# Kernel tuning notes

Measured on AMD Instinct MI355X. Metric: run time of the kernel, lower is better.

## Reference

```python
import jax, jax.numpy as jnp
import numpy as np
import math

D = 1024      # d_model
K = 64        # k_eigenstates
H = 4         # n_heads
KH = K // H   # eigenstates per head
MLP = 4 * D
B, T = 4, 4096


def setup_inputs() -> dict:
    key = jax.random.key(0)
    ks = jax.random.split(key, 16)
    rn = lambda k, shape, s: (jax.random.normal(k, shape, jnp.float32) * s)
    inp = {
        "x": rn(ks[0], (B, T, D), 1.0),
        "W_in": rn(ks[1], (2 * K, D), 1.0 / math.sqrt(D)),
        "log_decay": jax.random.uniform(ks[2], (K,), jnp.float32, -3.0, -0.1),
        "frequency": jnp.linspace(0.0, 2 * math.pi * (1 - 1.0 / K), K, dtype=jnp.float32),
        "W_sel": rn(ks[3], (2 * K, D), 0.01 / math.sqrt(D)),
        "b_sel": jnp.zeros((2 * K,), jnp.float32),
        "R": jnp.eye(KH, dtype=jnp.float32)[None] + 0.01 * rn(ks[4], (H, KH, KH), 1.0 / math.sqrt(KH)),
        "W_out": rn(ks[5], (D, 2 * K), 1.0 / math.sqrt(2 * K)),
        "W_g": rn(ks[6], (D, D), 1.0 / math.sqrt(D)),
        "b_g": jnp.full((D,), -2.0, jnp.float32),
        "g1": jnp.ones((D,), jnp.float32),
        "be1": jnp.zeros((D,), jnp.float32),
        "g2": jnp.ones((D,), jnp.float32),
        "be2": jnp.zeros((D,), jnp.float32),
        "W1": rn(ks[7], (MLP, D), 1.0 / math.sqrt(D)),
        "b1": jnp.zeros((MLP,), jnp.float32),
        "W2": rn(ks[8], (D, MLP), 1.0 / math.sqrt(MLP)),
        "b2": jnp.zeros((D,), jnp.float32),
    }
    return inp


def _ln(x, g, b):
    m = jnp.mean(x, axis=-1, keepdims=True)
    v = jnp.mean(jnp.square(x - m), axis=-1, keepdims=True)
    return (x - m) * jax.lax.rsqrt(v + 1e-5) * g + b


def _scan_combine(e1, e2):
    a1, b1 = e1
    a2, b2 = e2
    return a1 * a2, a2 * b1 + b2


def reference(x, W_in, log_decay, frequency, W_sel, b_sel, R, W_out, W_g, b_g,
              g1, be1, g2, be2, W1, b1, W2, b2):
    Bsz, Ts, Dm = x.shape
    residual = x
    x_norm = _ln(x, g1, be1)

    beta = x_norm @ W_in.T                      # [B,T,2K]
    beta_r, beta_i = jnp.split(beta, 2, axis=-1)

    delta = x_norm @ W_sel.T + b_sel            # selective modulation
    d_dec, d_fr = jnp.split(delta, 2, axis=-1)
    mag = jax.nn.sigmoid(log_decay + 0.1 * jnp.tanh(d_dec))   # [B,T,K]
    freq = frequency + 0.05 * jnp.tanh(d_fr)

    a = jax.lax.complex(mag * jnp.cos(freq), mag * jnp.sin(freq))  # lambda_t
    bc = jax.lax.complex(beta_r, beta_i)
    # inclusive prefix scan of c_t = a_t * c_{t-1} + b_t
    _, c = jax.lax.associative_scan(_scan_combine, (a, bc), axis=1)
    c_r, c_i = c.real, c.imag                   # [B,T,K]

    nH, Kh = R.shape[0], R.shape[1]
    c_r = jnp.einsum('hjk,bthk->bthj', R, c_r.reshape(Bsz, Ts, nH, Kh)).reshape(Bsz, Ts, -1)
    c_i = jnp.einsum('hjk,bthk->bthj', R, c_i.reshape(Bsz, Ts, nH, Kh)).reshape(Bsz, Ts, -1)

    h = jnp.concatenate([c_r, c_i], axis=-1) @ W_out.T
    gate = jax.nn.sigmoid(x_norm @ W_g.T + b_g)
    x = residual + gate * h

    x2 = _ln(x, g2, be2)
    x = x + (jax.nn.silu(x2 @ W1.T + b1) @ W2.T + b2)
    return x
```

## Files before the change

### kernel.cpp

```cpp
#include <hip/hip_runtime.h>
#include <math.h>

typedef __bf16 bf16_t;
typedef __attribute__((ext_vector_type(8))) __bf16 bf16x8;
typedef __attribute__((ext_vector_type(4))) float f32x4;

#define DMODEL 1024
#define NROWS  16384
#define SEQLEN 4096

static __device__ __forceinline__ float sigmoidf_(float v) { return 1.f / (1.f + __expf(-v)); }

#define GLOAD16(gsrc, ldst) __builtin_amdgcn_global_load_lds(                     \
    (const __attribute__((address_space(1))) void*)(gsrc),                        \
    (__attribute__((address_space(3))) void*)(ldst), 16, 0, 0)

__global__ __launch_bounds__(256) void ln_fused_kernel(const float* __restrict__ x,
                                                       const float* __restrict__ g,
                                                       const float* __restrict__ b,
                                                       bf16_t* __restrict__ out) {
  int row = blockIdx.x;
  int tid = threadIdx.x;
  const float4* xr = (const float4*)(x + (size_t)row * DMODEL);
  float4 v = xr[tid];
  float s  = v.x + v.y + v.z + v.w;
  float s2 = v.x*v.x + v.y*v.y + v.z*v.z + v.w*v.w;
  #pragma unroll
  for (int off = 32; off > 0; off >>= 1) {
    s  += __shfl_down(s, off);
    s2 += __shfl_down(s2, off);
  }
  __shared__ float sh[4], sh2[4];
  int lane = tid & 63, wid = tid >> 6;
  if (lane == 0) { sh[wid] = s; sh2[wid] = s2; }
  __syncthreads();
  s  = sh[0] + sh[1] + sh[2] + sh[3];
  s2 = sh2[0] + sh2[1] + sh2[2] + sh2[3];
  float m = s * (1.f / DMODEL);
  float var = fmaxf(s2 * (1.f / DMODEL) - m * m, 0.f);
  float rs = rsqrtf(var + 1e-5f);
  float4 gv = *(const float4*)&g[tid * 4];
  float4 bv = *(const float4*)&b[tid * 4];
  union { bf16_t h[4]; float2 f2; } u;
  u.h[0] = (bf16_t)((v.x - m) * rs * gv.x + bv.x);
  u.h[1] = (bf16_t)((v.y - m) * rs * gv.y + bv.y);
  u.h[2] = (bf16_t)((v.z - m) * rs * gv.z + bv.z);
  u.h[3] = (bf16_t)((v.w - m) * rs * gv.w + bv.w);
  *(float2*)&out[(size_t)row * DMODEL + tid * 4] = u.f2;
}

__global__ __launch_bounds__(256) void f32_to_bf16_kernel(const float* __restrict__ in,
                                                          bf16_t* __restrict__ out, int n) {
  int idx = (blockIdx.x * 256 + threadIdx.x) * 4;
  if (idx >= n) return;
  float4 v = *(const float4*)&in[idx];
  union { bf16_t h[4]; float2 f2; } u;
  u.h[0] = (bf16_t)v.x; u.h[1] = (bf16_t)v.y; u.h[2] = (bf16_t)v.z; u.h[3] = (bf16_t)v.w;
  *(float2*)&out[idx] = u.f2;
}

template<int EPI>
__global__ __launch_bounds__(512, 2) void gemm256_kernel(
    const bf16_t* __restrict__ A, int lda,
    const bf16_t* __restrict__ B, int ldb, int K, int nx,
    const float* __restrict__ bias,
    const float* __restrict__ res,
    const float* __restrict__ aux,
    float* __restrict__ outf, bf16_t* __restrict__ outb, int ldout) {
  __shared__ __align__(1024) char lds[2][2][32768];
  const int nwg = gridDim.x;
  const int bid = blockIdx.x;
  const int lid = (bid & 7) * (nwg >> 3) + (bid >> 3);
  const int n0 = (lid % nx) * 256;
  const int r0 = (lid / nx) * 256;

  const int tid = threadIdx.x;
  const int lane = tid & 63;
  const int w = tid >> 6;
  const int wr = w >> 2, wc = w & 3;
  const int fr = lane & 15;
  const int q16m = ((lane >> 4) * 16) ^ (((lane >> 2) & 1) << 5);
  const int srow = w * 8 + (lane >> 3);
  const int scolb = ((lane & 7) * 16) ^ (lane & 32);

  f32x4 acc[8][4];
  #pragma unroll
  for (int m = 0; m < 8; ++m)
    #pragma unroll
    for (int n = 0; n < 4; ++n) acc[m][n] = (f32x4){0.f, 0.f, 0.f, 0.f};

  const int nt = K >> 6;

  auto stage = [&](int d, int k0) {
    #pragma unroll
    for (int i = 0; i < 4; ++i) {
      GLOAD16((const char*)(A + (size_t)(r0 + i * 64 + srow) * lda + k0) + scolb,
              lds[d][0] + i * 8192 + w * 1024);
      GLOAD16((const char*)(B + (size_t)(n0 + i * 64 + srow) * ldb + k0) + scolb,
              lds[d][1] + i * 8192 + w * 1024);
    }
  };

  auto compute = [&](int d) {
    bf16x8 bfrag[4][2];
    #pragma unroll
    for (int n = 0; n < 4; ++n) {
      const char* bp = lds[d][1] + (wc * 64 + n * 16 + fr) * 128 + q16m;
      bfrag[n][0] = *(const bf16x8*)bp;
      bfrag[n][1] = *(const bf16x8*)(bp + 64);
    }
    #pragma unroll
    for (int mh = 0; mh < 2; ++mh) {
      bf16x8 afrag[4][2];
      #pragma unroll
      for (int m = 0; m < 4; ++m) {
        const char* ap = lds[d][0] + (wr * 128 + mh * 64 + m * 16 + fr) * 128 + q16m;
        afrag[m][0] = *(const bf16x8*)ap;
        afrag[m][1] = *(const bf16x8*)(ap + 64);
      }
      #pragma unroll
      for (int m = 0; m < 4; ++m)
        #pragma unroll
        for (int n = 0; n < 4; ++n) {
          acc[mh * 4 + m][n] = __builtin_amdgcn_mfma_f32_16x16x32_bf16(afrag[m][0], bfrag[n][0], acc[mh * 4 + m][n], 0, 0, 0);
          acc[mh * 4 + m][n] = __builtin_amdgcn_mfma_f32_16x16x32_bf16(afrag[m][1], bfrag[n][1], acc[mh * 4 + m][n], 0, 0, 0);
        }
    }
  };

  stage(0, 0);
  __syncthreads();
  for (int t = 0; t < nt; ++t) {
    if (t + 1 < nt) stage((t + 1) & 1, (t + 1) << 6);
    compute(t & 1);
    __syncthreads();
  }

  const int rbase = (lane >> 4) * 4;
  #pragma unroll
  for (int mf = 0; mf < 8; ++mf) {
    #pragma unroll
    for (int n = 0; n < 4; ++n) {
      int row = r0 + wr * 128 + mf * 16 + rbase;
      int col = n0 + wc * 64 + n * 16 + fr;
      f32x4 v = acc[mf][n];
      #pragma unroll
      for (int j = 0; j < 4; ++j) {
        int r = row + j;
        float val = v[j];
        if (EPI == 0) {
          outf[(size_t)r * ldout + col] = val;
        } else if (EPI == 1) {
          float t2 = val + bias[col];
          t2 = t2 * sigmoidf_(t2);
          outb[(size_t)r * ldout + col] = (bf16_t)t2;
        } else if (EPI == 2) {
          outf[(size_t)r * ldout + col] = res[(size_t)r * 1024 + col] + bias[col] + val;
        } else if (EPI == 3) {
          outf[(size_t)r * ldout + col] += val;
        } else {
          size_t idx = (size_t)r * 1024 + col;
          outf[idx] = res[idx] + sigmoidf_(val + bias[col]) * aux[idx];
        }
      }
    }
  }
}

template<int EPI>
__global__ __launch_bounds__(256) void gemm_bf16_kernel(
    const bf16_t* __restrict__ A, int lda,
    const bf16_t* __restrict__ B, int ldb, int K, int nx,
    float* __restrict__ outf, int ldout) {
  __shared__ __align__(16) bf16_t As[128 * 32];
  __shared__ __align__(16) bf16_t Bs[128 * 32];
  const int nwg = gridDim.x;
  const int bid = blockIdx.x;
  const int lid = (bid & 7) * (nwg >> 3) + (bid >> 3);
  const int n0 = (lid % nx) * 128;
  const int r0 = (lid / nx) * 128;

  const int tid = threadIdx.x;
  const int lane = tid & 63;
  const int w = tid >> 6;
  const int wr = w >> 1, wc = w & 1;
  const int srow0 = tid >> 2;
  const int srow1 = 64 + (tid >> 2);
  const int skk = (tid & 3) * 8;
  const int fr = lane & 15;
  const int ko = (lane >> 4) * 8;

  f32x4 acc[4][4];
  #pragma unroll
  for (int m = 0; m < 4; ++m)
    #pragma unroll
    for (int n = 0; n < 4; ++n) acc[m][n] = (f32x4){0.f, 0.f, 0.f, 0.f};

  for (int k0 = 0; k0 < K; k0 += 32) {
    GLOAD16(A + (size_t)(r0 + srow0) * lda + k0 + skk, (char*)As + w * 1024);
    GLOAD16(A + (size_t)(r0 + srow1) * lda + k0 + skk, (char*)As + 4096 + w * 1024);
    GLOAD16(B + (size_t)(n0 + srow0) * ldb + k0 + skk, (char*)Bs + w * 1024);
    GLOAD16(B + (size_t)(n0 + srow1) * ldb + k0 + skk, (char*)Bs + 4096 + w * 1024);
    __syncthreads();
    bf16x8 af[4], bfr[4];
    #pragma unroll
    for (int m = 0; m < 4; ++m)
      af[m] = *(const bf16x8*)&As[(wr * 64 + m * 16 + fr) * 32 + ko];
    #pragma unroll
    for (int n = 0; n < 4; ++n)
      bfr[n] = *(const bf16x8*)&Bs[(wc * 64 + n * 16 + fr) * 32 + ko];
    #pragma unroll
    for (int m = 0; m < 4; ++m)
      #pragma unroll
      for (int n = 0; n < 4; ++n)
        acc[m][n] = __builtin_amdgcn_mfma_f32_16x16x32_bf16(af[m], bfr[n], acc[m][n], 0, 0, 0);
    __syncthreads();
  }

  const int rbase = (lane >> 4) * 4;
  #pragma unroll
  for (int m = 0; m < 4; ++m) {
    #pragma unroll
    for (int n = 0; n < 4; ++n) {
      int row = r0 + wr * 64 + m * 16 + rbase;
      int col = n0 + wc * 64 + n * 16 + fr;
      f32x4 v = acc[m][n];
      #pragma unroll
      for (int j = 0; j < 4; ++j)
        outf[(size_t)(row + j) * ldout + col] = v[j];
    }
  }
}

__global__ __launch_bounds__(256) void ew_ab_kernel(
    const float* __restrict__ bd, const float* __restrict__ b_sel,
    const float* __restrict__ log_decay, const float* __restrict__ frequency,
    float* __restrict__ a_r, float* __restrict__ a_i,
    float* __restrict__ b_r, float* __restrict__ b_i) {
  __shared__ float T[32][257];
  int bb = blockIdx.x >> 7;
  int t0 = (blockIdx.x & 127) << 5;
  int tid = threadIdx.x;
  #pragma unroll
  for (int p = 0; p < 32; ++p) {
    int idx = tid + p * 256;
    int tt = idx >> 8, j = idx & 255;
    T[tt][j] = bd[((size_t)bb * 4096 + t0 + tt) * 256 + j];
  }
  __syncthreads();
  #pragma unroll
  for (int p = 0; p < 8; ++p) {
    int idx = tid + p * 256;
    int tt = idx & 31, k = idx >> 5;
    float br_ = T[tt][k];
    float bi_ = T[tt][64 + k];
    float dd = T[tt][128 + k] + b_sel[k];
    float df = T[tt][192 + k] + b_sel[64 + k];
    float mag = sigmoidf_(log_decay[k] + 0.1f * tanhf(dd));
    float fr = frequency[k] + 0.05f * tanhf(df);
    float ar_ = mag * cosf(fr), ai_ = mag * sinf(fr);
    size_t o = ((size_t)bb * 64 + k) * 4096 + t0 + tt;
    a_r[o] = ar_; a_i[o] = ai_; b_r[o] = br_; b_i[o] = bi_;
  }
}

__global__ __launch_bounds__(256) void scan_kernel(
    const float* __restrict__ a_r, const float* __restrict__ a_i,
    const float* b_r, const float* b_i,
    float* c_r, float* c_i) {
  int seq = blockIdx.x;
  size_t base = (size_t)seq * SEQLEN;
  int tid = threadIdx.x;
  int t0 = tid * 16;
  float Ar = 1.f, Ai = 0.f, Br = 0.f, Bi = 0.f;
  #pragma unroll
  for (int s = 0; s < 16; ++s) {
    size_t t = base + t0 + s;
    float ar = a_r[t], ai = a_i[t], br = b_r[t], bi = b_i[t];
    float nBr = ar * Br - ai * Bi + br;
    float nBi = ar * Bi + ai * Br + bi;
    Br = nBr; Bi = nBi;
    float nAr = ar * Ar - ai * Ai;
    float nAi = ar * Ai + ai * Ar;
    Ar = nAr; Ai = nAi;
  }
  __shared__ float sAr[256], sAi[256], sBr[256], sBi[256];
  sAr[tid] = Ar; sAi[tid] = Ai; sBr[tid] = Br; sBi[tid] = Bi;
  for (int off = 1; off < 256; off <<= 1) {
    __syncthreads();
    float pAr = 0.f, pAi = 0.f, pBr = 0.f, pBi = 0.f;
    if (tid >= off) { pAr = sAr[tid - off]; pAi = sAi[tid - off]; pBr = sBr[tid - off]; pBi = sBi[tid - off]; }
    __syncthreads();
    if (tid >= off) {
      float cAr = sAr[tid], cAi = sAi[tid], cBr = sBr[tid], cBi = sBi[tid];
      float nBr = cAr * pBr - cAi * pBi + cBr;
      float nBi = cAr * pBi + cAi * pBr + cBi;
      float nAr = cAr * pAr - cAi * pAi;
      float nAi = cAr * pAi + cAi * pAr;
      sAr[tid] = nAr; sAi[tid] = nAi; sBr[tid] = nBr; sBi[tid] = nBi;
    }
  }
  __syncthreads();
  float cr = (tid > 0) ? sBr[tid - 1] : 0.f;
  float ci = (tid > 0) ? sBi[tid - 1] : 0.f;
  #pragma unroll
  for (int s = 0; s < 16; ++s) {
    size_t t = base + t0 + s;
    float ar = a_r[t], ai = a_i[t], br = b_r[t], bi = b_i[t];
    float nr = ar * cr - ai * ci + br;
    float ni = ar * ci + ai * cr + bi;
    cr = nr; ci = ni;
    c_r[t] = cr; c_i[t] = ci;
  }
}

__global__ __launch_bounds__(256) void transpose_cc_kernel(
    const float* __restrict__ c_r, const float* __restrict__ c_i,
    bf16_t* __restrict__ cc) {
  __shared__ float Tr[64][65];
  __shared__ float Ti[64][65];
  int t0 = blockIdx.x * 64;
  int bb = blockIdx.y;
  int tid = threadIdx.x;
  int tt = tid & 63;
  int q = tid >> 6;
  #pragma unroll
  for (int p = 0; p < 16; ++p) {
    int k = p * 4 + q;
    size_t src = ((size_t)bb * 64 + k) * 4096 + t0 + tt;
    Tr[tt][k] = c_r[src];
    Ti[tt][k] = c_i[src];
  }
  __syncthreads();
  #pragma unroll
  for (int p = 0; p < 16; ++p) {
    int tt2 = p * 4 + q;
    int k = tid & 63;
    size_t row = (size_t)bb * 4096 + t0 + tt2;
    cc[row * 128 + k] = (bf16_t)Tr[tt2][k];
    cc[row * 128 + 64 + k] = (bf16_t)Ti[tt2][k];
  }
}

__global__ __launch_bounds__(256) void weff_kernel(const float* __restrict__ W_out,
                                                   const float* __restrict__ R,
                                                   bf16_t* __restrict__ Weff) {
  int idx = blockIdx.x * 256 + threadIdx.x;
  int d = idx >> 7, col = idx & 127;
  int k = col & 63, h = k >> 4, kk = k & 15;
  int off = (col < 64) ? 0 : 64;
  float s = 0.f;
  #pragma unroll
  for (int j = 0; j < 16; ++j)
    s += W_out[d * 128 + off + h * 16 + j] * R[h * 256 + j * 16 + kk];
  Weff[idx] = (bf16_t)s;
}

extern "C" void kernel_launch(void* const* d_in, const int* in_sizes, int n_in,
                              void* d_out, int out_size, void* d_ws, size_t ws_size,
                              hipStream_t stream) {
  (void)in_sizes; (void)n_in; (void)out_size; (void)ws_size;
  const float* x         = (const float*)d_in[0];
  const float* W_in      = (const float*)d_in[1];
  const float* log_decay = (const float*)d_in[2];
  const float* frequency = (const float*)d_in[3];
  const float* W_sel     = (const float*)d_in[4];
  const float* b_sel     = (const float*)d_in[5];
  const float* R         = (const float*)d_in[6];
  const float* W_out     = (const float*)d_in[7];
  const float* W_g       = (const float*)d_in[8];
  const float* b_g       = (const float*)d_in[9];
  const float* g1        = (const float*)d_in[10];
  const float* be1       = (const float*)d_in[11];
  const float* g2        = (const float*)d_in[12];
  const float* be2       = (const float*)d_in[13];
  const float* W1        = (const float*)d_in[14];
  const float* b1        = (const float*)d_in[15];
  const float* W2        = (const float*)d_in[16];
  const float* b2        = (const float*)d_in[17];
  float* out = (float*)d_out;
  float* ws  = (float*)d_ws;

  const size_t M1 = (size_t)1 << 20;
  float* bd   = ws;
  float* xmid = ws;
  float* a_r  = ws + 16 * M1;
  float* a_i  = ws + 20 * M1;
  float* b_rr = ws + 24 * M1;
  float* b_ii = ws + 28 * M1;
  float* hbuf = ws + 16 * M1;
  bf16_t* mid = (bf16_t*)(ws + 16 * M1);
  bf16_t* xn  = (bf16_t*)(ws + 32 * M1);
  bf16_t* cc  = (bf16_t*)(ws + 40 * M1);
  bf16_t* Wbd = (bf16_t*)(ws + 41 * M1);
  bf16_t* Wgb = (bf16_t*)(ws + 41 * M1 + (128 << 10));
  bf16_t* W1b = (bf16_t*)(ws + 41 * M1 + (640 << 10));
  bf16_t* W2b = (bf16_t*)(ws + 43 * M1 + (640 << 10));
  bf16_t* Wef = (bf16_t*)(ws + 45 * M1 + (640 << 10));

  dim3 blk(256);
  dim3 blk512(512);

  ln_fused_kernel<<<NROWS, blk, 0, stream>>>(x, g1, be1, xn);

  f32_to_bf16_kernel<<<128, blk, 0, stream>>>(W_in, Wbd, 128 * 1024);
  f32_to_bf16_kernel<<<128, blk, 0, stream>>>(W_sel, Wbd + 128 * 1024, 128 * 1024);
  f32_to_bf16_kernel<<<1024, blk, 0, stream>>>(W_g, Wgb, 1024 * 1024);
  f32_to_bf16_kernel<<<4096, blk, 0, stream>>>(W1, W1b, 4 * 1024 * 1024);
  f32_to_bf16_kernel<<<4096, blk, 0, stream>>>(W2, W2b, 4 * 1024 * 1024);
  weff_kernel<<<512, blk, 0, stream>>>(W_out, R, Wef);

  gemm_bf16_kernel<0><<<256, blk, 0, stream>>>(xn, 1024, Wbd, 1024, 1024, 2, bd, 256);

  ew_ab_kernel<<<512, blk, 0, stream>>>(bd, b_sel, log_decay, frequency, a_r, a_i, b_rr, b_ii);
  scan_kernel<<<256, blk, 0, stream>>>(a_r, a_i, b_rr, b_ii, b_rr, b_ii);
  transpose_cc_kernel<<<dim3(64, 4), blk, 0, stream>>>(b_rr, b_ii, cc);

  gemm256_kernel<0><<<256, blk512, 0, stream>>>(
      cc, 128, Wef, 128, 128, 4, nullptr, nullptr, nullptr, hbuf, nullptr, 1024);

  gemm256_kernel<4><<<256, blk512, 0, stream>>>(
      xn, 1024, Wgb, 1024, 1024, 4, b_g, x, hbuf, xmid, nullptr, 1024);

  ln_fused_kernel<<<NROWS, blk, 0, stream>>>(xmid, g2, be2, xn);

  for (int h = 0; h < 2; ++h) {
    gemm256_kernel<1><<<512, blk512, 0, stream>>>(
        xn, 1024, W1b + (size_t)h * 2048 * 1024, 1024, 1024, 8,
        b1 + h * 2048, nullptr, nullptr, nullptr, mid, 2048);
    if (h == 0) {
      gemm256_kernel<2><<<256, blk512, 0, stream>>>(
          mid, 2048, W2b, 4096, 2048, 4,
          b2, xmid, nullptr, out, nullptr, 1024);
    } else {
      gemm256_kernel<3><<<256, blk512, 0, stream>>>(
          mid, 2048, W2b + 2048, 4096, 2048, 4,
          nullptr, nullptr, nullptr, out, nullptr, 1024);
    }
  }
}
```

Before: 545.0 us.

## Pipeline bf16 GEMM mainloop into four prioritized phases with interleaved LDS staging

Replaces the simple double-buffered stage/compute loop of the 256x256 bf16 GEMM with a four-phase schedule. Each phase loads one A or B quarter-fragment from LDS, issues the next tile's global-to-LDS loads for a freed half, then runs a block of MFMAs at raised wave priority between barriers. Explicit vmcnt/lgkmcnt waits replace the full __syncthreads per tile. The LDS layout and XOR swizzle are also reorganised into per-half buffers. This aims to overlap global loads, LDS reads and MFMA work more finely, at the cost of more barriers and fragile hand-tuned wait counts.

Result: faster. 527.0 us (-3.3%).

```diff
diff --git a/kernel.cpp b/kernel.cpp
--- a/kernel.cpp
+++ b/kernel.cpp
@@ -59,6 +59,43 @@
   *(float2*)&out[idx] = u.f2;
 }
 
+#define LOADA(d, mh)                                                              \
+  { _Pragma("unroll")                                                             \
+    for (int m_ = 0; m_ < 4; ++m_) {                                              \
+      _Pragma("unroll")                                                           \
+      for (int kk_ = 0; kk_ < 2; ++kk_)                                           \
+        afrag[m_][kk_] = *(const bf16x8*)(ldsp + (d) * 32768 + (mh) * 16384 +     \
+            (aRow + m_ * 16) * 128 + ((kk_ * 64 + q16) ^ swz));                   \
+    } }
+
+#define LOADB(d, nn)                                                              \
+  { _Pragma("unroll")                                                             \
+    for (int n2_ = 0; n2_ < 2; ++n2_) {                                           \
+      _Pragma("unroll")                                                           \
+      for (int kk_ = 0; kk_ < 2; ++kk_)                                           \
+        bfrag[nn][n2_][kk_] = *(const bf16x8*)(ldsp + 65536 + (d) * 32768 +       \
+            (nn) * 16384 + (bRow + n2_ * 16) * 128 + ((kk_ * 64 + q16) ^ swz));   \
+    } }
+
+#define MFMAQ(mh, nn)                                                             \
+  { _Pragma("unroll")                                                             \
+    for (int m_ = 0; m_ < 4; ++m_) {                                              \
+      _Pragma("unroll")                                                           \
+      for (int n2_ = 0; n2_ < 2; ++n2_) {                                         \
+        acc[(mh)*4+m_][(nn)*2+n2_] = __builtin_amdgcn_mfma_f32_16x16x32_bf16(     \
+            afrag[m_][0], bfrag[nn][n2_][0], acc[(mh)*4+m_][(nn)*2+n2_], 0,0,0);  \
+        acc[(mh)*4+m_][(nn)*2+n2_] = __builtin_amdgcn_mfma_f32_16x16x32_bf16(     \
+            afrag[m_][1], bfrag[nn][n2_][1], acc[(mh)*4+m_][(nn)*2+n2_], 0,0,0);  \
+      }                                                                           \
+    } }
+
+#define PH_PRE()  __builtin_amdgcn_s_barrier();                                   \
+                  asm volatile("s_waitcnt lgkmcnt(0)");                           \
+                  __builtin_amdgcn_sched_barrier(0);                              \
+                  __builtin_amdgcn_s_setprio(1)
+#define PH_POST() __builtin_amdgcn_s_setprio(0);                                  \
+                  __builtin_amdgcn_s_barrier()
+
 template<int EPI>
 __global__ __launch_bounds__(512, 2) void gemm256_kernel(
     const bf16_t* __restrict__ A, int lda,
@@ -67,7 +104,7 @@
     const float* __restrict__ res,
     const float* __restrict__ aux,
     float* __restrict__ outf, bf16_t* __restrict__ outb, int ldout) {
-  __shared__ __align__(1024) char lds[2][2][32768];
+  __shared__ __align__(128) char ldsp[131072];
   const int nwg = gridDim.x;
   const int bid = blockIdx.x;
   const int lid = (bid & 7) * (nwg >> 3) + (bid >> 3);
@@ -79,61 +116,87 @@
   const int w = tid >> 6;
   const int wr = w >> 2, wc = w & 3;
   const int fr = lane & 15;
-  const int q16m = ((lane >> 4) * 16) ^ (((lane >> 2) & 1) << 5);
-  const int srow = w * 8 + (lane >> 3);
-  const int scolb = ((lane & 7) * 16) ^ (lane & 32);
+  const int q16 = (lane >> 4) * 16;
+  const int swz = (fr & 7) << 4;
+  const int aRow = wr * 64 + fr;
+  const int bRow = wc * 32 + fr;
+
+  const size_t lda_b = (size_t)lda * 2;
+  const size_t ldb_b = (size_t)ldb * 2;
+  const char* Ab = (const char*)A;
+  const char* Bb = (const char*)B;
+  const int trow = tid >> 3;
+  const int scolb = (((tid & 7) ^ (trow & 7)) << 4);
+
+  auto stageA = [&](int d, int h, int kt) {
+    const char* src = Ab + (size_t)(r0 + h * 64 + trow) * lda_b + kt * 128 + scolb;
+    char* dst = ldsp + d * 32768 + h * 16384 + tid * 16;
+    GLOAD16(src, dst);
+    GLOAD16(src + 128 * lda_b, dst + 8192);
+  };
+  auto stageB = [&](int d, int g, int kt) {
+    const int r1 = 64 + trow;
+    const char* s0 = Bb + (size_t)(n0 + (trow >> 5) * 64 + g * 32 + (trow & 31)) * ldb_b + kt * 128 + scolb;
+    const char* s1 = Bb + (size_t)(n0 + (r1 >> 5) * 64 + g * 32 + (r1 & 31)) * ldb_b + kt * 128 + scolb;
+    char* dst = ldsp + 65536 + d * 32768 + g * 16384 + tid * 16;
+    GLOAD16(s0, dst);
+    GLOAD16(s1, dst + 8192);
+  };
 
   f32x4 acc[8][4];
   #pragma unroll
   for (int m = 0; m < 8; ++m)
     #pragma unroll
     for (int n = 0; n < 4; ++n) acc[m][n] = (f32x4){0.f, 0.f, 0.f, 0.f};
+  bf16x8 afrag[4][2];
+  bf16x8 bfrag[2][2][2];
 
   const int nt = K >> 6;
 
-  auto stage = [&](int d, int k0) {
-    #pragma unroll
-    for (int i = 0; i < 4; ++i) {
-      GLOAD16((const char*)(A + (size_t)(r0 + i * 64 + srow) * lda + k0) + scolb,
-              lds[d][0] + i * 8192 + w * 1024);
-      GLOAD16((const char*)(B + (size_t)(n0 + i * 64 + srow) * ldb + k0) + scolb,
-              lds[d][1] + i * 8192 + w * 1024);
-    }
-  };
-
-  auto compute = [&](int d) {
-    bf16x8 bfrag[4][2];
-    #pragma unroll
-    for (int n = 0; n < 4; ++n) {
-      const char* bp = lds[d][1] + (wc * 64 + n * 16 + fr) * 128 + q16m;
-      bfrag[n][0] = *(const bf16x8*)bp;
-      bfrag[n][1] = *(const bf16x8*)(bp + 64);
-    }
-    #pragma unroll
-    for (int mh = 0; mh < 2; ++mh) {
-      bf16x8 afrag[4][2];
-      #pragma unroll
-      for (int m = 0; m < 4; ++m) {
-        const char* ap = lds[d][0] + (wr * 128 + mh * 64 + m * 16 + fr) * 128 + q16m;
-        afrag[m][0] = *(const bf16x8*)ap;
-        afrag[m][1] = *(const bf16x8*)(ap + 64);
-      }
-      #pragma unroll
-      for (int m = 0; m < 4; ++m)
-        #pragma unroll
-        for (int n = 0; n < 4; ++n) {
-          acc[mh * 4 + m][n] = __builtin_amdgcn_mfma_f32_16x16x32_bf16(afrag[m][0], bfrag[n][0], acc[mh * 4 + m][n], 0, 0, 0);
-          acc[mh * 4 + m][n] = __builtin_amdgcn_mfma_f32_16x16x32_bf16(afrag[m][1], bfrag[n][1], acc[mh * 4 + m][n], 0, 0, 0);
-        }
-    }
-  };
-
-  stage(0, 0);
-  __syncthreads();
-  for (int t = 0; t < nt; ++t) {
-    if (t + 1 < nt) stage((t + 1) & 1, (t + 1) << 6);
-    compute(t & 1);
-    __syncthreads();
+  stageA(0, 0, 0); stageB(0, 0, 0); stageB(0, 1, 0); stageA(0, 1, 0);
+  if (nt > 1) {
+    stageA(1, 0, 1); stageB(1, 0, 1); stageB(1, 1, 1);
+    asm volatile("s_waitcnt vmcnt(6)");
+  } else {
+    asm volatile("s_waitcnt vmcnt(0)");
+  }
+  __builtin_amdgcn_s_barrier();
+
+  for (int t = 0; t < nt - 1; ++t) {
+    const int d = t & 1, dn = d ^ 1;
+    LOADA(d, 0) LOADB(d, 0)
+    stageA(dn, 1, t + 1);
+    PH_PRE(); MFMAQ(0, 0) PH_POST();
+    LOADB(d, 1)
+    if (t + 2 < nt) stageA(d, 0, t + 2);
+    PH_PRE(); MFMAQ(0, 1) PH_POST();
+    LOADA(d, 1)
+    if (t + 2 < nt) stageB(d, 0, t + 2);
+    PH_PRE(); MFMAQ(1, 0) PH_POST();
+    if (t + 2 < nt) stageB(d, 1, t + 2);
+    __builtin_amdgcn_s_barrier();
+    __builtin_amdgcn_s_setprio(1);
+    MFMAQ(1, 1)
+    __builtin_amdgcn_s_setprio(0);
+    if (t == nt - 2) { asm volatile("s_waitcnt vmcnt(0)"); }
+    else             { asm volatile("s_waitcnt vmcnt(6)"); }
+    __builtin_amdgcn_s_barrier();
+  }
+  {
+    const int d = (nt - 1) & 1;
+    LOADA(d, 0) LOADB(d, 0)
+    asm volatile("s_waitcnt lgkmcnt(0)");
+    __builtin_amdgcn_sched_barrier(0);
+    MFMAQ(0, 0)
+    LOADB(d, 1)
+    asm volatile("s_waitcnt lgkmcnt(0)");
+    __builtin_amdgcn_sched_barrier(0);
+    MFMAQ(0, 1)
+    LOADA(d, 1)
+    asm volatile("s_waitcnt lgkmcnt(0)");
+    __builtin_amdgcn_sched_barrier(0);
+    MFMAQ(1, 0)
+    MFMAQ(1, 1)
   }
 
   const int rbase = (lane >> 4) * 4;
```

## Shrink GEMM tile to 128x256 single-buffered, bf16 h buffer, unsplit MLP

Applied to the files above, without the earlier changes.

Replaces the 256x256 double-buffered GEMM with a 128x256 single-buffered tile that uses 48KB of LDS and an XOR swizzle, allowing 4 workgroups per CU to hide latency through occupancy instead of software pipelining. The intermediate h output is now written as bf16 instead of f32, which halves that traffic. When the workspace is large enough, the MLP runs as one full-width W1 GEMM and one W2 GEMM instead of two halves with a read-modify-write accumulate. The costs are less reuse per tile, a barrier-exposed load every K step, and reduced precision for h.

Measured after the change: 476.7 us. -12.5%, faster.

```diff
diff --git a/kernel.cpp b/kernel.cpp
--- a/kernel.cpp
+++ b/kernel.cpp
@@ -60,88 +60,78 @@
 }
 
 template<int EPI>
-__global__ __launch_bounds__(512, 2) void gemm256_kernel(
+__global__ __launch_bounds__(512, 4) void gemmB_kernel(
     const bf16_t* __restrict__ A, int lda,
     const bf16_t* __restrict__ B, int ldb, int K, int nx,
     const float* __restrict__ bias,
     const float* __restrict__ res,
-    const float* __restrict__ aux,
+    const bf16_t* __restrict__ auxb,
     float* __restrict__ outf, bf16_t* __restrict__ outb, int ldout) {
-  __shared__ __align__(1024) char lds[2][2][32768];
+  __shared__ __align__(128) bf16_t Asm[128 * 64];
+  __shared__ __align__(128) bf16_t Bsm[256 * 64];
   const int nwg = gridDim.x;
   const int bid = blockIdx.x;
   const int lid = (bid & 7) * (nwg >> 3) + (bid >> 3);
   const int n0 = (lid % nx) * 256;
-  const int r0 = (lid / nx) * 256;
+  const int r0 = (lid / nx) * 128;
 
   const int tid = threadIdx.x;
   const int lane = tid & 63;
   const int w = tid >> 6;
   const int wr = w >> 2, wc = w & 3;
   const int fr = lane & 15;
-  const int q16m = ((lane >> 4) * 16) ^ (((lane >> 2) & 1) << 5);
-  const int srow = w * 8 + (lane >> 3);
-  const int scolb = ((lane & 7) * 16) ^ (lane & 32);
-
-  f32x4 acc[8][4];
-  #pragma unroll
-  for (int m = 0; m < 8; ++m)
+  const int q16 = (lane >> 4) * 16;
+  const int swz = (fr & 7) << 4;
+  const int trow = tid >> 3;
+  const int scolb = ((tid & 7) ^ (trow & 7)) << 4;
+
+  const size_t lda_b = (size_t)lda * 2;
+  const size_t ldb_b = (size_t)ldb * 2;
+  const char* Ab = (const char*)A;
+  const char* Bb = (const char*)B;
+  char* lA = (char*)Asm;
+  char* lB = (char*)Bsm;
+
+  f32x4 acc[4][4];
+  #pragma unroll
+  for (int m = 0; m < 4; ++m)
     #pragma unroll
     for (int n = 0; n < 4; ++n) acc[m][n] = (f32x4){0.f, 0.f, 0.f, 0.f};
 
-  const int nt = K >> 6;
-
-  auto stage = [&](int d, int k0) {
-    #pragma unroll
-    for (int i = 0; i < 4; ++i) {
-      GLOAD16((const char*)(A + (size_t)(r0 + i * 64 + srow) * lda + k0) + scolb,
-              lds[d][0] + i * 8192 + w * 1024);
-      GLOAD16((const char*)(B + (size_t)(n0 + i * 64 + srow) * ldb + k0) + scolb,
-              lds[d][1] + i * 8192 + w * 1024);
-    }
-  };
-
-  auto compute = [&](int d) {
-    bf16x8 bfrag[4][2];
-    #pragma unroll
-    for (int n = 0; n < 4; ++n) {
-      const char* bp = lds[d][1] + (wc * 64 + n * 16 + fr) * 128 + q16m;
-      bfrag[n][0] = *(const bf16x8*)bp;
-      bfrag[n][1] = *(const bf16x8*)(bp + 64);
-    }
-    #pragma unroll
-    for (int mh = 0; mh < 2; ++mh) {
-      bf16x8 afrag[4][2];
-      #pragma unroll
-      for (int m = 0; m < 4; ++m) {
-        const char* ap = lds[d][0] + (wr * 128 + mh * 64 + m * 16 + fr) * 128 + q16m;
-        afrag[m][0] = *(const bf16x8*)ap;
-        afrag[m][1] = *(const bf16x8*)(ap + 64);
-      }
+  for (int kt = 0; kt < K; kt += 64) {
+    const char* sa = Ab + (size_t)(r0 + trow) * lda_b + kt * 2 + scolb;
+    GLOAD16(sa, lA + tid * 16);
+    GLOAD16(sa + 64 * lda_b, lA + 8192 + tid * 16);
+    const char* sb = Bb + (size_t)(n0 + trow) * ldb_b + kt * 2 + scolb;
+    GLOAD16(sb, lB + tid * 16);
+    GLOAD16(sb + 64 * ldb_b,  lB + 8192  + tid * 16);
+    GLOAD16(sb + 128 * ldb_b, lB + 16384 + tid * 16);
+    GLOAD16(sb + 192 * ldb_b, lB + 24576 + tid * 16);
+    __syncthreads();
+    #pragma unroll
+    for (int kh = 0; kh < 2; ++kh) {
+      bf16x8 af[4], bv[4];
+      #pragma unroll
+      for (int m = 0; m < 4; ++m)
+        af[m] = *(const bf16x8*)(lA + (wr * 64 + m * 16 + fr) * 128 + ((kh * 64 + q16) ^ swz));
+      #pragma unroll
+      for (int n = 0; n < 4; ++n)
+        bv[n] = *(const bf16x8*)(lB + (wc * 64 + n * 16 + fr) * 128 + ((kh * 64 + q16) ^ swz));
       #pragma unroll
       for (int m = 0; m < 4; ++m)
         #pragma unroll
-        for (int n = 0; n < 4; ++n) {
-          acc[mh * 4 + m][n] = __builtin_amdgcn_mfma_f32_16x16x32_bf16(afrag[m][0], bfrag[n][0], acc[mh * 4 + m][n], 0, 0, 0);
-          acc[mh * 4 + m][n] = __builtin_amdgcn_mfma_f32_16x16x32_bf16(afrag[m][1], bfrag[n][1], acc[mh * 4 + m][n], 0, 0, 0);
-        }
+        for (int n = 0; n < 4; ++n)
+          acc[m][n] = __builtin_amdgcn_mfma_f32_16x16x32_bf16(af[m], bv[n], acc[m][n], 0, 0, 0);
     }
-  };
-
-  stage(0, 0);
-  __syncthreads();
-  for (int t = 0; t < nt; ++t) {
-    if (t + 1 < nt) stage((t + 1) & 1, (t + 1) << 6);
-    compute(t & 1);
     __syncthreads();
   }
 
   const int rbase = (lane >> 4) * 4;
   #pragma unroll
-  for (int mf = 0; mf < 8; ++mf) {
+  for (int mf = 0; mf < 4; ++mf) {
     #pragma unroll
     for (int n = 0; n < 4; ++n) {
-      int row = r0 + wr * 128 + mf * 16 + rbase;
+      int row = r0 + wr * 64 + mf * 16 + rbase;
       int col = n0 + wc * 64 + n * 16 + fr;
       f32x4 v = acc[mf][n];
       #pragma unroll
@@ -158,9 +148,11 @@
           outf[(size_t)r * ldout + col] = res[(size_t)r * 1024 + col] + bias[col] + val;
         } else if (EPI == 3) {
           outf[(size_t)r * ldout + col] += val;
+        } else if (EPI == 4) {
+          size_t idx = (size_t)r * 1024 + col;
+          outf[idx] = res[idx] + sigmoidf_(val + bias[col]) * (float)auxb[idx];
         } else {
-          size_t idx = (size_t)r * 1024 + col;
-          outf[idx] = res[idx] + sigmoidf_(val + bias[col]) * aux[idx];
+          outb[(size_t)r * ldout + col] = (bf16_t)val;
         }
       }
     }
@@ -359,7 +351,7 @@
 extern "C" void kernel_launch(void* const* d_in, const int* in_sizes, int n_in,
                               void* d_out, int out_size, void* d_ws, size_t ws_size,
                               hipStream_t stream) {
-  (void)in_sizes; (void)n_in; (void)out_size; (void)ws_size;
+  (void)in_sizes; (void)n_in; (void)out_size;
   const float* x         = (const float*)d_in[0];
   const float* W_in      = (const float*)d_in[1];
   const float* log_decay = (const float*)d_in[2];
@@ -382,21 +374,26 @@
   float* ws  = (float*)d_ws;
 
   const size_t M1 = (size_t)1 << 20;
+  const bool full = ws_size >= (size_t)62 * M1 * sizeof(float);
+
   float* bd   = ws;
   float* xmid = ws;
   float* a_r  = ws + 16 * M1;
   float* a_i  = ws + 20 * M1;
   float* b_rr = ws + 24 * M1;
   float* b_ii = ws + 28 * M1;
-  float* hbuf = ws + 16 * M1;
+  bf16_t* hbufb = (bf16_t*)(ws + 16 * M1);
   bf16_t* mid = (bf16_t*)(ws + 16 * M1);
-  bf16_t* xn  = (bf16_t*)(ws + 32 * M1);
-  bf16_t* cc  = (bf16_t*)(ws + 40 * M1);
-  bf16_t* Wbd = (bf16_t*)(ws + 41 * M1);
-  bf16_t* Wgb = (bf16_t*)(ws + 41 * M1 + (128 << 10));
-  bf16_t* W1b = (bf16_t*)(ws + 41 * M1 + (640 << 10));
-  bf16_t* W2b = (bf16_t*)(ws + 43 * M1 + (640 << 10));
-  bf16_t* Wef = (bf16_t*)(ws + 45 * M1 + (640 << 10));
+  size_t wx = full ? 48 * M1 : 32 * M1;
+  size_t wc_off = full ? 56 * M1 : 40 * M1;
+  size_t wb = full ? 57 * M1 : 41 * M1;
+  bf16_t* xn  = (bf16_t*)(ws + wx);
+  bf16_t* cc  = (bf16_t*)(ws + wc_off);
+  bf16_t* Wbd = (bf16_t*)(ws + wb);
+  bf16_t* Wgb = (bf16_t*)(ws + wb + (128 << 10));
+  bf16_t* W1b = (bf16_t*)(ws + wb + (640 << 10));
+  bf16_t* W2b = (bf16_t*)(ws + wb + 2 * M1 + (640 << 10));
+  bf16_t* Wef = (bf16_t*)(ws + wb + 4 * M1 + (640 << 10));
 
   dim3 blk(256);
   dim3 blk512(512);
@@ -416,26 +413,31 @@
   scan_kernel<<<256, blk, 0, stream>>>(a_r, a_i, b_rr, b_ii, b_rr, b_ii);
   transpose_cc_kernel<<<dim3(64, 4), blk, 0, stream>>>(b_rr, b_ii, cc);
 
-  gemm256_kernel<0><<<256, blk512, 0, stream>>>(
-      cc, 128, Wef, 128, 128, 4, nullptr, nullptr, nullptr, hbuf, nullptr, 1024);
-
-  gemm256_kernel<4><<<256, blk512, 0, stream>>>(
-      xn, 1024, Wgb, 1024, 1024, 4, b_g, x, hbuf, xmid, nullptr, 1024);
+  gemmB_kernel<5><<<512, blk512, 0, stream>>>(
+      cc, 128, Wef, 128, 128, 4, nullptr, nullptr, nullptr, nullptr, hbufb, 1024);
+
+  gemmB_kernel<4><<<512, blk512, 0, stream>>>(
+      xn, 1024, Wgb, 1024, 1024, 4, b_g, x, hbufb, xmid, nullptr, 1024);
 
   ln_fused_kernel<<<NROWS, blk, 0, stream>>>(xmid, g2, be2, xn);
 
-  for (int h = 0; h < 2; ++h) {
-    gemm256_kernel<1><<<512, blk512, 0, stream>>>(
-        xn, 1024, W1b + (size_t)h * 2048 * 1024, 1024, 1024, 8,
-        b1 + h * 2048, nullptr, nullptr, nullptr, mid, 2048);
-    if (h == 0) {
-      gemm256_kernel<2><<<256, blk512, 0, stream>>>(
-          mid, 2048, W2b, 4096, 2048, 4,
-          b2, xmid, nullptr, out, nullptr, 1024);
-    } else {
-      gemm256_kernel<3><<<256, blk512, 0, stream>>>(
-          mid, 2048, W2b + 2048, 4096, 2048, 4,
-          nullptr, nullptr, nullptr, out, nullptr, 1024);
+  if (full) {
+    gemmB_kernel<1><<<2048, blk512, 0, stream>>>(
+        xn, 1024, W1b, 1024, 1024, 16, b1, nullptr, nullptr, nullptr, mid, 4096);
+    gemmB_kernel<2><<<512, blk512, 0, stream>>>(
+        mid, 4096, W2b, 4096, 4096, 4, b2, xmid, nullptr, out, nullptr, 1024);
+  } else {
+    for (int h = 0; h < 2; ++h) {
+      gemmB_kernel<1><<<1024, blk512, 0, stream>>>(
+          xn, 1024, W1b + (size_t)h * 2048 * 1024, 1024, 1024, 8,
+          b1 + h * 2048, nullptr, nullptr, nullptr, mid, 2048);
+      if (h == 0) {
+        gemmB_kernel<2><<<512, blk512, 0, stream>>>(
+            mid, 2048, W2b, 4096, 2048, 4, b2, xmid, nullptr, out, nullptr, 1024);
+      } else {
+        gemmB_kernel<3><<<512, blk512, 0, stream>>>(
+            mid, 2048, W2b + 2048, 4096, 2048, 4, nullptr, nullptr, nullptr, out, nullptr, 1024);
+      }
     }
   }
 }
```
